# Kernel tuning notes

Measured on AMD Instinct MI355X. Metric: run time of the kernel, lower is better.

## Reference

```python
import jax, jax.numpy as jnp
import numpy as np

EPS = 1e-12  # F.normalize default eps


def setup_inputs() -> dict:
    key = jax.random.key(0)
    k1, k2, k3, k4 = jax.random.split(key, 4)
    B, N, C, NH = 8, 4096, 512, 8
    x = jax.random.normal(k1, (B, N, C), dtype=jnp.float32)
    Wqkv = jax.random.normal(k2, (3 * C, C), dtype=jnp.float32) * 0.02
    Wproj = jax.random.normal(k3, (C, C), dtype=jnp.float32) * 0.02
    bproj = jax.random.normal(k4, (C,), dtype=jnp.float32) * 0.01
    temp = jnp.ones((NH, 1, 1), dtype=jnp.float32)
    return {"x": x, "Wqkv": Wqkv, "Wproj": Wproj, "bproj": bproj,
            "temp": temp, "H": 64, "W": 64}


def _l2norm(t):
    # normalize along last axis, matching F.normalize(p=2, eps=1e-12)
    return t / jnp.maximum(jnp.linalg.norm(t, axis=-1, keepdims=True), EPS)


def reference(x, Wqkv, Wproj, bproj, temp, H, W):
    B, N, C = x.shape
    nh = temp.shape[0]
    hd = C // nh
    # qkv projection: [B, N, 3, nh, hd]
    qkv = jnp.einsum('bnc,dc->bnd', x, Wqkv).reshape(B, N, 3, nh, hd)
    q = qkv[:, :, 0]  # [B, N, nh, hd]
    k = qkv[:, :, 1]
    v = qkv[:, :, 2]
    # transpose to [B, nh, hd, N] and L2-normalize along tokens (N)
    qn = _l2norm(q.transpose(0, 2, 3, 1))
    kn = _l2norm(k.transpose(0, 2, 3, 1))
    vt = v.transpose(0, 2, 3, 1)  # [B, nh, hd, N]
    # channel attention: [B, nh, hd, hd], scaled by learned per-head temp
    attn = jax.nn.softmax(jnp.einsum('bhcn,bhdn->bhcd', qn, kn) * temp, axis=-1)
    # [B, nh, hd, N] -> [B, N, nh, hd] -> [B, N, C]
    out = jnp.einsum('bhcd,bhdn->bhcn', attn, vt).transpose(0, 3, 1, 2).reshape(B, N, C)
    return jnp.einsum('bnc,dc->bnd', out, Wproj) + bproj
```

## Files before the change

### kernel.cpp

```cpp
#include <hip/hip_runtime.h>
#include <stdint.h>

#define DEVI __device__ __forceinline__

typedef __attribute__((ext_vector_type(8))) short bf16x8;
typedef __attribute__((ext_vector_type(4))) float f32x4;
typedef __attribute__((ext_vector_type(4))) unsigned short u16x4;
typedef __attribute__((ext_vector_type(4))) float float4v;

DEVI unsigned short f2bf(float f) {
  unsigned int u = __builtin_bit_cast(unsigned int, f);
  u += 0x7FFFu + ((u >> 16) & 1u);
  return (unsigned short)(u >> 16);
}
DEVI float bf2f(short s) {
  unsigned int u = ((unsigned int)(unsigned short)s) << 16;
  return __builtin_bit_cast(float, u);
}
DEVI void gload16(const unsigned short* g, unsigned short* l) {
  __builtin_amdgcn_global_load_lds(
      (const __attribute__((address_space(1))) unsigned int*)g,
      (__attribute__((address_space(3))) unsigned int*)l, 16, 0, 0);
}

__global__ void cast_prep(const float* __restrict__ x,
                          unsigned short* __restrict__ Xbf,
                          unsigned short* __restrict__ xT,
                          const float* __restrict__ Wqkv,
                          unsigned short* __restrict__ Wqk,
                          unsigned short* __restrict__ WvT) {
  __shared__ float tls[64 * 129];
  const int t = threadIdx.x;
  if (blockIdx.z < 8) {
    const int n0 = blockIdx.x * 128, c0 = blockIdx.y * 64, b = blockIdx.z;
    const int q = t & 15;
    const int nl = t >> 4;
#pragma unroll
    for (int i = 0; i < 8; ++i) {
      const int n = i * 16 + nl;
      const size_t gi = ((size_t)b * 4096 + n0 + n) * 512 + c0 + q * 4;
      float4v f = *(const float4v*)&x[gi];
      u16x4 o;
      o.x = f2bf(f.x); o.y = f2bf(f.y); o.z = f2bf(f.z); o.w = f2bf(f.w);
      *(u16x4*)&Xbf[gi] = o;
      tls[(q * 4 + 0) * 129 + n] = f.x;
      tls[(q * 4 + 1) * 129 + n] = f.y;
      tls[(q * 4 + 2) * 129 + n] = f.z;
      tls[(q * 4 + 3) * 129 + n] = f.w;
    }
    __syncthreads();
    const int cr = t >> 2, nq = t & 3;
#pragma unroll
    for (int ii = 0; ii < 4; ++ii) {
      const int n = nq * 8 + ii * 32;
      bf16x8 o;
#pragma unroll
      for (int s = 0; s < 8; ++s) o[s] = (short)f2bf(tls[cr * 129 + n + s]);
      *(bf16x8*)&xT[((size_t)b * 512 + c0 + cr) * 4096 + n0 + n] = o;
    }
    return;
  }
  const int id = blockIdx.y * 32 + blockIdx.x;
  {
    const float4v* src = (const float4v*)Wqkv;
    u16x4* dst = (u16x4*)Wqk;
    int base = id * 512 + t;
#pragma unroll
    for (int j = 0; j < 2; ++j) {
      int i = base + j * 256;
      float4v f = src[i];
      u16x4 o;
      o.x = f2bf(f.x); o.y = f2bf(f.y); o.z = f2bf(f.z); o.w = f2bf(f.w);
      dst[i] = o;
    }
  }
  if (id < 64) {
    const int tr = id >> 3, tc = id & 7;
    const int c = t & 63, rb = t >> 6;
    __syncthreads();
#pragma unroll
    for (int rr = 0; rr < 16; ++rr) {
      int r = rb * 16 + rr;
      tls[r * 65 + c] = Wqkv[(size_t)(1024 + tr * 64 + r) * 512 + tc * 64 + c];
    }
    __syncthreads();
#pragma unroll
    for (int rr = 0; rr < 16; ++rr) {
      int j = rb * 16 + rr;
      WvT[(size_t)(tc * 64 + j) * 512 + tr * 64 + c] = f2bf(tls[c * 65 + j]);
    }
  }
}

template <int KITERS>
DEVI void gemm_db(const unsigned short* gA, int strideA,
                  const unsigned short* gB, int strideB,
                  unsigned short (*lA)[4096], unsigned short (*lB)[4096],
                  int wave, int wr, int wc, int fr, int kg, f32x4 acc[4][4]) {
  const int wo = wave * 512;
#define STAGE_T(buf, kk)                                                    \
  gload16(gA + (kk) * 32, lA[buf] + wo);                                    \
  gload16(gA + (kk) * 32 + (size_t)64 * strideA, lA[buf] + wo + 2048);      \
  gload16(gB + (kk) * 32, lB[buf] + wo);                                    \
  gload16(gB + (kk) * 32 + (size_t)64 * strideB, lB[buf] + wo + 2048);
  STAGE_T(0, 0);
  __syncthreads();
  int cur = 0;
  for (int kk = 1; kk <= KITERS; ++kk) {
    if (kk < KITERS) { STAGE_T(cur ^ 1, kk); }
    bf16x8 af[4], bfv[4];
#pragma unroll
    for (int mi = 0; mi < 4; ++mi)
      af[mi] = *(const bf16x8*)&lA[cur][(wr * 64 + mi * 16 + fr) * 32 + kg * 8];
#pragma unroll
    for (int ni = 0; ni < 4; ++ni)
      bfv[ni] = *(const bf16x8*)&lB[cur][(wc * 64 + ni * 16 + fr) * 32 + kg * 8];
#pragma unroll
    for (int mi = 0; mi < 4; ++mi)
#pragma unroll
      for (int ni = 0; ni < 4; ++ni)
        acc[mi][ni] = __builtin_amdgcn_mfma_f32_16x16x32_bf16(
            af[mi], bfv[ni], acc[mi][ni], 0, 0, 0);
    __syncthreads();
    cur ^= 1;
  }
#undef STAGE_T
}

__launch_bounds__(256)
__global__ void gsyrk(const unsigned short* __restrict__ xT,
                      unsigned short* __restrict__ Gpart) {
  __shared__ __align__(16) unsigned short lA[2][4096];
  __shared__ __align__(16) unsigned short lB[2][4096];
  static const int PTC[10] = {0, 0, 0, 0, 1, 1, 1, 2, 2, 3};
  static const int PTD[10] = {0, 1, 2, 3, 1, 2, 3, 2, 3, 3};
  const int tid = threadIdx.x, wave = tid >> 6, lane = tid & 63;
  const int wr = wave >> 1, wc = wave & 1, fr = lane & 15, kg = lane >> 4;
  const int tc = PTC[blockIdx.x], td = PTD[blockIdx.x];
  const int chunk = blockIdx.y, b = blockIdx.z;
  const unsigned short* xb = xT + (size_t)b * 512 * 4096 + chunk * 512;
  f32x4 acc[4][4] = {};
  const int sRow = wave * 16 + (lane >> 2);
  const int sK = (lane & 3) * 8;
  gemm_db<16>(xb + (size_t)(tc * 128 + sRow) * 4096 + sK, 4096,
              xb + (size_t)(td * 128 + sRow) * 4096 + sK, 4096,
              lA, lB, wave, wr, wc, fr, kg, acc);
  unsigned short* Gp = Gpart + (size_t)(chunk * 8 + b) * 512 * 512;
#pragma unroll
  for (int mi = 0; mi < 4; ++mi) {
    const int rIT = wr * 64 + mi * 16 + kg * 4;
#pragma unroll
    for (int ni = 0; ni < 4; ++ni) {
      const int cIT = wc * 64 + ni * 16 + fr;
      f32x4 v = acc[mi][ni];
#pragma unroll
      for (int r = 0; r < 4; ++r)
        Gp[(size_t)(tc * 128 + rIT + r) * 512 + td * 128 + cIT] = f2bf(v[r]);
      if (tc != td) {
        u16x4 o;
        o.x = f2bf(v[0]); o.y = f2bf(v[1]); o.z = f2bf(v[2]); o.w = f2bf(v[3]);
        *(u16x4*)&Gp[(size_t)(td * 128 + cIT) * 512 + tc * 128 + rIT] = o;
      }
    }
  }
}

__global__ void greduce(const unsigned short* __restrict__ Gpart,
                        unsigned short* __restrict__ Gbf) {
  const int stride = gridDim.x * blockDim.x;
  const int n4 = 8 * 512 * 512 / 4;
  for (int i = blockIdx.x * blockDim.x + threadIdx.x; i < n4; i += stride) {
    const int b = i >> 16, j4 = i & 65535;
    float s0 = 0, s1 = 0, s2 = 0, s3 = 0;
#pragma unroll
    for (int c = 0; c < 8; ++c) {
      u16x4 v = ((const u16x4*)Gpart)[(size_t)(c * 8 + b) * 65536 + j4];
      s0 += bf2f((short)v.x); s1 += bf2f((short)v.y);
      s2 += bf2f((short)v.z); s3 += bf2f((short)v.w);
    }
    u16x4 o;
    o.x = f2bf(s0); o.y = f2bf(s1); o.z = f2bf(s2); o.w = f2bf(s3);
    ((u16x4*)Gbf)[i] = o;
  }
}

__launch_bounds__(256)
__global__ void tall_gemm(const unsigned short* __restrict__ Wqk,
                          const unsigned short* __restrict__ Gbf,
                          unsigned short* __restrict__ Tbf,
                          float* __restrict__ ssPart) {
  __shared__ __align__(16) unsigned short lA[2][4096];
  __shared__ __align__(16) unsigned short lB[2][4096];
  __shared__ float ssL[128][2];
  const int tid = threadIdx.x, wave = tid >> 6, lane = tid & 63;
  const int wr = wave >> 1, wc = wave & 1, fr = lane & 15, kg = lane >> 4;
  const int rowBase = blockIdx.x * 128, colBase = blockIdx.y * 128;
  const int b = blockIdx.z;
  const unsigned short* Gb = Gbf + (size_t)b * 512 * 512;
  f32x4 acc[4][4] = {};
  const int sRow = wave * 16 + (lane >> 2);
  const int sK = (lane & 3) * 8;
  gemm_db<16>(Wqk + (size_t)(rowBase + sRow) * 512 + sK, 512,
              Gb + (size_t)(colBase + sRow) * 512 + sK, 512,
              lA, lB, wave, wr, wc, fr, kg, acc);
  unsigned short* Tb = Tbf + (size_t)b * 1024 * 512;
#pragma unroll
  for (int mi = 0; mi < 4; ++mi) {
    const int rbase = rowBase + wr * 64 + mi * 16 + kg * 4;
    f32x4 sacc = {0.f, 0.f, 0.f, 0.f};
#pragma unroll
    for (int ni = 0; ni < 4; ++ni) {
      const int col = colBase + wc * 64 + ni * 16 + fr;
      f32x4 v = acc[mi][ni];
#pragma unroll
      for (int r = 0; r < 4; ++r) {
        float w = bf2f((short)Wqk[(size_t)(rbase + r) * 512 + col]);
        Tb[(size_t)(rbase + r) * 512 + col] = f2bf(v[r]);
        sacc[r] += v[r] * w;
      }
    }
#pragma unroll
    for (int o = 1; o < 16; o <<= 1) {
#pragma unroll
      for (int r = 0; r < 4; ++r) sacc[r] += __shfl_xor(sacc[r], o);
    }
    if (fr == 0) {
#pragma unroll
      for (int r = 0; r < 4; ++r)
        ssL[wr * 64 + mi * 16 + kg * 4 + r][wc] = sacc[r];
    }
  }
  __syncthreads();
  if (tid < 128)
    ssPart[((size_t)blockIdx.y * 8 + b) * 1024 + rowBase + tid] =
        ssL[tid][0] + ssL[tid][1];
}

__global__ void s_softmax(const unsigned short* __restrict__ Tbf,
                          const unsigned short* __restrict__ Wqk,
                          const float* __restrict__ ssPart,
                          const float* __restrict__ temp,
                          float* __restrict__ attnOut) {
  __shared__ float Sl[64 * 64];
  __shared__ float invq[64], invk[64];
  const int bh = blockIdx.x, b = bh >> 3, h = bh & 7;
  const unsigned short* qbase = Tbf + (size_t)(b * 1024 + h * 64) * 512;
  const unsigned short* kbase = Wqk + (size_t)(512 + h * 64) * 512;
  const int t = threadIdx.x;
  const int wave = t >> 6, lane = t & 63;
  const int wr = wave >> 1, wc = wave & 1, fr = lane & 15, kg = lane >> 4;
  f32x4 acc[2][2] = {};
  for (int kk = 0; kk < 512; kk += 32) {
    bf16x8 a[2], bb[2];
#pragma unroll
    for (int mi = 0; mi < 2; ++mi)
      a[mi] = *(const bf16x8*)(qbase + (size_t)(wr * 32 + mi * 16 + fr) * 512 + kk + kg * 8);
#pragma unroll
    for (int ni = 0; ni < 2; ++ni)
      bb[ni] = *(const bf16x8*)(kbase + (size_t)(wc * 32 + ni * 16 + fr) * 512 + kk + kg * 8);
#pragma unroll
    for (int mi = 0; mi < 2; ++mi)
#pragma unroll
      for (int ni = 0; ni < 2; ++ni)
        acc[mi][ni] = __builtin_amdgcn_mfma_f32_16x16x32_bf16(a[mi], bb[ni], acc[mi][ni], 0, 0, 0);
  }
#pragma unroll
  for (int mi = 0; mi < 2; ++mi)
#pragma unroll
    for (int ni = 0; ni < 2; ++ni) {
      f32x4 v = acc[mi][ni];
#pragma unroll
      for (int r = 0; r < 4; ++r)
        Sl[(wr * 32 + mi * 16 + kg * 4 + r) * 64 + wc * 32 + ni * 16 + fr] = v[r];
    }
  if (t < 128) {
    const int r = (t >> 6) * 512 + h * 64 + (t & 63);
    float s = 0.f;
#pragma unroll
    for (int nt = 0; nt < 4; ++nt) s += ssPart[((size_t)nt * 8 + b) * 1024 + r];
    float inv = 1.f / fmaxf(sqrtf(s), 1e-12f);
    if (t < 64) invq[t] = inv;
    else invk[t - 64] = inv;
  }
  __syncthreads();
  const float tmp = temp[h];
  const int c = t >> 2, q4 = t & 3;
  float lg[16];
  float mx = -1e30f;
#pragma unroll
  for (int j = 0; j < 16; ++j) {
    const int d = q4 * 16 + j;
    lg[j] = Sl[c * 64 + d] * invq[c] * invk[d] * tmp;
    mx = fmaxf(mx, lg[j]);
  }
  mx = fmaxf(mx, __shfl_xor(mx, 1));
  mx = fmaxf(mx, __shfl_xor(mx, 2));
  float sum = 0.f;
#pragma unroll
  for (int j = 0; j < 16; ++j) {
    lg[j] = __expf(lg[j] - mx);
    sum += lg[j];
  }
  sum += __shfl_xor(sum, 1);
  sum += __shfl_xor(sum, 2);
  const float inv = 1.f / sum;
#pragma unroll
  for (int j = 0; j < 16; ++j)
    attnOut[(size_t)bh * 4096 + c * 64 + q4 * 16 + j] = lg[j] * inv;
}

__global__ void weff_kernel(const float* __restrict__ attn,
                            const float* __restrict__ Wproj,
                            unsigned short* __restrict__ Weff) {
  const int bh = blockIdx.x, eb = blockIdx.y;
  const int b = bh >> 3, h = bh & 7;
  __shared__ float at[64 * 64];
  for (int i = threadIdx.x; i < 4096; i += 256)
    at[i] = attn[(size_t)bh * 4096 + i];
  __syncthreads();
  const int e = eb * 64 + (threadIdx.x >> 2);
  const int dq = threadIdx.x & 3;
  float acc[16] = {};
  const float* wrow = Wproj + (size_t)e * 512 + h * 64;
  for (int c = 0; c < 64; ++c) {
    const float w = wrow[c];
#pragma unroll
    for (int j = 0; j < 16; ++j) acc[j] += w * at[c * 64 + dq * 16 + j];
  }
  unsigned short* outp = Weff + ((size_t)b * 512 + e) * 512 + h * 64 + dq * 16;
#pragma unroll
  for (int j = 0; j < 16; ++j) outp[j] = f2bf(acc[j]);
}

__launch_bounds__(256)
__global__ void wcomb_gemm(const unsigned short* __restrict__ WeffAll,
                           const unsigned short* __restrict__ WvT,
                           unsigned short* __restrict__ WcombAll) {
  __shared__ __align__(16) unsigned short lA[2][4096];
  __shared__ __align__(16) unsigned short lB[2][4096];
  const int tid = threadIdx.x, wave = tid >> 6, lane = tid & 63;
  const int wr = wave >> 1, wc = wave & 1, fr = lane & 15, kg = lane >> 4;
  const int b = blockIdx.z;
  const int rowBase = blockIdx.x * 128, colBase = blockIdx.y * 128;
  const unsigned short* A = WeffAll + (size_t)b * 512 * 512;
  f32x4 acc[4][4] = {};
  const int sRow = wave * 16 + (lane >> 2);
  const int sK = (lane & 3) * 8;
  gemm_db<16>(A + (size_t)(rowBase + sRow) * 512 + sK, 512,
              WvT + (size_t)(colBase + sRow) * 512 + sK, 512,
              lA, lB, wave, wr, wc, fr, kg, acc);
  unsigned short* Wc = WcombAll + (size_t)b * 512 * 512;
#pragma unroll
  for (int mi = 0; mi < 4; ++mi) {
    const int rbase = rowBase + wr * 64 + mi * 16 + kg * 4;
#pragma unroll
    for (int ni = 0; ni < 4; ++ni) {
      const int col = colBase + wc * 64 + ni * 16 + fr;
      f32x4 v = acc[mi][ni];
#pragma unroll
      for (int r = 0; r < 4; ++r)
        Wc[(size_t)(rbase + r) * 512 + col] = f2bf(v[r]);
    }
  }
}

__launch_bounds__(256)
__global__ void out_gemm(const unsigned short* __restrict__ Xbf,
                         const unsigned short* __restrict__ WcombAll,
                         const float* __restrict__ bias,
                         float* __restrict__ out) {
  __shared__ __align__(16) unsigned short lA[2][4096];
  __shared__ __align__(16) unsigned short lB[2][4096];
  const int tid = threadIdx.x, wave = tid >> 6, lane = tid & 63;
  const int wr = wave >> 1, wc = wave & 1, fr = lane & 15, kg = lane >> 4;
  const int b = blockIdx.z;
  const int rowBase = blockIdx.x * 128, colBase = blockIdx.y * 128;
  const unsigned short* A = Xbf + (size_t)b * 4096 * 512;
  const unsigned short* Bw = WcombAll + (size_t)b * 512 * 512;
  f32x4 acc[4][4] = {};
  const int sRow = wave * 16 + (lane >> 2);
  const int sK = (lane & 3) * 8;
  gemm_db<16>(A + (size_t)(rowBase + sRow) * 512 + sK, 512,
              Bw + (size_t)(colBase + sRow) * 512 + sK, 512,
              lA, lB, wave, wr, wc, fr, kg, acc);
#pragma unroll
  for (int mi = 0; mi < 4; ++mi) {
    const int rbase = rowBase + wr * 64 + mi * 16 + kg * 4;
#pragma unroll
    for (int ni = 0; ni < 4; ++ni) {
      const int col = colBase + wc * 64 + ni * 16 + fr;
      const float bcol = bias[col];
      f32x4 v = acc[mi][ni];
#pragma unroll
      for (int r = 0; r < 4; ++r)
        out[((size_t)b * 4096 + rbase + r) * 512 + col] = v[r] + bcol;
    }
  }
}

extern "C" void kernel_launch(void* const* d_in, const int* in_sizes, int n_in,
                              void* d_out, int out_size, void* d_ws, size_t ws_size,
                              hipStream_t stream) {
  const float* x = (const float*)d_in[0];
  const float* Wqkv = (const float*)d_in[1];
  const float* Wproj = (const float*)d_in[2];
  const float* bproj = (const float*)d_in[3];
  const float* temp = (const float*)d_in[4];
  float* out = (float*)d_out;

  char* ws = (char*)d_ws;
  unsigned short* Xbf = (unsigned short*)(ws + 0);
  unsigned short* xT = (unsigned short*)(ws + 33554432);
  unsigned short* Wqk = (unsigned short*)(ws + 67108864);
  unsigned short* WvT = (unsigned short*)(ws + 68157440);
  unsigned short* Gpart = (unsigned short*)(ws + 68681728);
  unsigned short* Gbf = (unsigned short*)(ws + 102236160);
  unsigned short* Tbf = (unsigned short*)(ws + 106430464);
  float* ssPart = (float*)(ws + 114819072);
  float* attn = (float*)(ws + 114950144);
  unsigned short* Weff = (unsigned short*)(ws + 115998720);
  unsigned short* Wcomb = (unsigned short*)(ws + 120193024);

  cast_prep<<<dim3(32, 8, 9), 256, 0, stream>>>(x, Xbf, xT, Wqkv, Wqk, WvT);
  gsyrk<<<dim3(10, 8, 8), 256, 0, stream>>>(xT, Gpart);
  greduce<<<1024, 256, 0, stream>>>(Gpart, Gbf);
  tall_gemm<<<dim3(8, 4, 8), 256, 0, stream>>>(Wqk, Gbf, Tbf, ssPart);
  s_softmax<<<64, 256, 0, stream>>>(Tbf, Wqk, ssPart, temp, attn);
  weff_kernel<<<dim3(64, 8), 256, 0, stream>>>(attn, Wproj, Weff);
  wcomb_gemm<<<dim3(4, 4, 8), 256, 0, stream>>>(Weff, WvT, Wcomb);
  out_gemm<<<dim3(32, 4, 8), 256, 0, stream>>>(Xbf, Wcomb, bproj, out);
}
```

Baseline: 143.0 us.

## Use 256x256 swizzled-LDS GEMM tiles for gsyrk and out_gemm

Adds a shared 256x256-tile, 8-wave GEMM loop with K=64 stages, an XOR-swizzled LDS layout, explicit vmcnt waits and MFMA priority hints. gsyrk and out_gemm now use it. gsyrk drops the symmetric 10-tile triangle scheme and computes all four 256 tiles. The larger tiles raise data reuse per block and the swizzle cuts LDS bank conflicts, but grids shrink to 256 blocks and gsyrk now does redundant work on the symmetric half.

After: 130.4 us. 8.8% less time.

```diff
diff --git a/kernel.cpp b/kernel.cpp
--- a/kernel.cpp
+++ b/kernel.cpp
@@ -89,6 +89,122 @@
       int j = rb * 16 + rr;
       WvT[(size_t)(tc * 64 + j) * 512 + tr * 64 + c] = f2bf(tls[c * 65 + j]);
     }
+  }
+}
+
+#define STAGE256(kt)                                                         \
+  {                                                                          \
+    const int bo_ = ((kt) & 1) * 16384;                                      \
+    _Pragma("unroll") for (int i_ = 0; i_ < 4; ++i_) {                       \
+      gload16(pA + (size_t)i_ * 64 * strideA + (kt) * 64,                    \
+              ldsA + bo_ + i_ * 4096 + wave * 512);                          \
+      gload16(pB + (size_t)i_ * 64 * strideB + (kt) * 64,                    \
+              ldsB + bo_ + i_ * 4096 + wave * 512);                          \
+    }                                                                        \
+  }
+
+template <int NT>
+DEVI void gemm256_loop(const unsigned short* pA, size_t strideA,
+                       const unsigned short* pB, size_t strideB,
+                       unsigned short* ldsA, unsigned short* ldsB,
+                       int wave, int lane, f32x4 acc[8][4]) {
+  const int wr = wave >> 2, wc = wave & 3;
+  const int fr = lane & 15, kg = lane >> 4;
+  const int x0 = ((kg * 16) ^ ((fr & 7) << 4)) >> 1;
+  const int x1 = ((64 + kg * 16) ^ ((fr & 7) << 4)) >> 1;
+  STAGE256(0);
+  for (int kt = 0; kt < NT; ++kt) {
+    __builtin_amdgcn_s_barrier();
+    __builtin_amdgcn_sched_barrier(0);
+    if (kt + 1 < NT) {
+      STAGE256(kt + 1);
+      asm volatile("s_waitcnt vmcnt(8)" ::: "memory");
+    } else {
+      asm volatile("s_waitcnt vmcnt(0)" ::: "memory");
+    }
+    __builtin_amdgcn_sched_barrier(0);
+    __builtin_amdgcn_s_barrier();
+    __builtin_amdgcn_sched_barrier(0);
+    const int bo = (kt & 1) * 16384;
+    bf16x8 bfrag[4][2];
+#pragma unroll
+    for (int n = 0; n < 4; ++n) {
+      const int ro = (wc * 64 + n * 16 + fr) * 64;
+      bfrag[n][0] = *(const bf16x8*)&ldsB[bo + ro + x0];
+      bfrag[n][1] = *(const bf16x8*)&ldsB[bo + ro + x1];
+    }
+#pragma unroll
+    for (int mp = 0; mp < 4; ++mp) {
+      bf16x8 af[2][2];
+#pragma unroll
+      for (int mi = 0; mi < 2; ++mi) {
+        const int ro = (wr * 128 + (mp * 2 + mi) * 16 + fr) * 64;
+        af[mi][0] = *(const bf16x8*)&ldsA[bo + ro + x0];
+        af[mi][1] = *(const bf16x8*)&ldsA[bo + ro + x1];
+      }
+      __builtin_amdgcn_s_setprio(1);
+#pragma unroll
+      for (int mi = 0; mi < 2; ++mi)
+#pragma unroll
+        for (int n = 0; n < 4; ++n) {
+          acc[mp * 2 + mi][n] = __builtin_amdgcn_mfma_f32_16x16x32_bf16(
+              af[mi][0], bfrag[n][0], acc[mp * 2 + mi][n], 0, 0, 0);
+          acc[mp * 2 + mi][n] = __builtin_amdgcn_mfma_f32_16x16x32_bf16(
+              af[mi][1], bfrag[n][1], acc[mp * 2 + mi][n], 0, 0, 0);
+        }
+      __builtin_amdgcn_s_setprio(0);
+    }
+  }
+}
+
+__launch_bounds__(512, 2)
+__global__ void gsyrk(const unsigned short* __restrict__ xT,
+                      unsigned short* __restrict__ Gpart) {
+  __shared__ __align__(16) unsigned short ldsA[2 * 16384];
+  __shared__ __align__(16) unsigned short ldsB[2 * 16384];
+  const int tid = threadIdx.x, wave = tid >> 6, lane = tid & 63;
+  const int tc = blockIdx.x >> 1, td = blockIdx.x & 1;
+  const int chunk = blockIdx.y, b = blockIdx.z;
+  const unsigned short* xb = xT + (size_t)b * 512 * 4096 + chunk * 512;
+  const int sRow = tid >> 3;
+  const int kEl = 8 * ((tid & 7) ^ ((tid >> 3) & 7));
+  const unsigned short* pA = xb + (size_t)(tc * 256 + sRow) * 4096 + kEl;
+  const unsigned short* pB = xb + (size_t)(td * 256 + sRow) * 4096 + kEl;
+  f32x4 acc[8][4] = {};
+  gemm256_loop<8>(pA, 4096, pB, 4096, ldsA, ldsB, wave, lane, acc);
+  const int wr = wave >> 2, wc = wave & 3;
+  const int fr = lane & 15, kg = lane >> 4;
+  unsigned short* Gp = Gpart + (size_t)(chunk * 8 + b) * 512 * 512;
+#pragma unroll
+  for (int m = 0; m < 8; ++m) {
+    const int row0 = tc * 256 + wr * 128 + m * 16 + kg * 4;
+#pragma unroll
+    for (int n = 0; n < 4; ++n) {
+      const int col = td * 256 + wc * 64 + n * 16 + fr;
+      f32x4 v = acc[m][n];
+#pragma unroll
+      for (int r = 0; r < 4; ++r)
+        Gp[(size_t)(row0 + r) * 512 + col] = f2bf(v[r]);
+    }
+  }
+}
+
+__global__ void greduce(const unsigned short* __restrict__ Gpart,
+                        unsigned short* __restrict__ Gbf) {
+  const int stride = gridDim.x * blockDim.x;
+  const int n4 = 8 * 512 * 512 / 4;
+  for (int i = blockIdx.x * blockDim.x + threadIdx.x; i < n4; i += stride) {
+    const int b = i >> 16, j4 = i & 65535;
+    float s0 = 0, s1 = 0, s2 = 0, s3 = 0;
+#pragma unroll
+    for (int c = 0; c < 8; ++c) {
+      u16x4 v = ((const u16x4*)Gpart)[(size_t)(c * 8 + b) * 65536 + j4];
+      s0 += bf2f((short)v.x); s1 += bf2f((short)v.y);
+      s2 += bf2f((short)v.z); s3 += bf2f((short)v.w);
+    }
+    u16x4 o;
+    o.x = f2bf(s0); o.y = f2bf(s1); o.z = f2bf(s2); o.w = f2bf(s3);
+    ((u16x4*)Gbf)[i] = o;
   }
 }
 
@@ -125,63 +241,6 @@
     cur ^= 1;
   }
 #undef STAGE_T
-}
-
-__launch_bounds__(256)
-__global__ void gsyrk(const unsigned short* __restrict__ xT,
-                      unsigned short* __restrict__ Gpart) {
-  __shared__ __align__(16) unsigned short lA[2][4096];
-  __shared__ __align__(16) unsigned short lB[2][4096];
-  static const int PTC[10] = {0, 0, 0, 0, 1, 1, 1, 2, 2, 3};
-  static const int PTD[10] = {0, 1, 2, 3, 1, 2, 3, 2, 3, 3};
-  const int tid = threadIdx.x, wave = tid >> 6, lane = tid & 63;
-  const int wr = wave >> 1, wc = wave & 1, fr = lane & 15, kg = lane >> 4;
-  const int tc = PTC[blockIdx.x], td = PTD[blockIdx.x];
-  const int chunk = blockIdx.y, b = blockIdx.z;
-  const unsigned short* xb = xT + (size_t)b * 512 * 4096 + chunk * 512;
-  f32x4 acc[4][4] = {};
-  const int sRow = wave * 16 + (lane >> 2);
-  const int sK = (lane & 3) * 8;
-  gemm_db<16>(xb + (size_t)(tc * 128 + sRow) * 4096 + sK, 4096,
-              xb + (size_t)(td * 128 + sRow) * 4096 + sK, 4096,
-              lA, lB, wave, wr, wc, fr, kg, acc);
-  unsigned short* Gp = Gpart + (size_t)(chunk * 8 + b) * 512 * 512;
-#pragma unroll
-  for (int mi = 0; mi < 4; ++mi) {
-    const int rIT = wr * 64 + mi * 16 + kg * 4;
-#pragma unroll
-    for (int ni = 0; ni < 4; ++ni) {
-      const int cIT = wc * 64 + ni * 16 + fr;
-      f32x4 v = acc[mi][ni];
-#pragma unroll
-      for (int r = 0; r < 4; ++r)
-        Gp[(size_t)(tc * 128 + rIT + r) * 512 + td * 128 + cIT] = f2bf(v[r]);
-      if (tc != td) {
-        u16x4 o;
-        o.x = f2bf(v[0]); o.y = f2bf(v[1]); o.z = f2bf(v[2]); o.w = f2bf(v[3]);
-        *(u16x4*)&Gp[(size_t)(td * 128 + cIT) * 512 + tc * 128 + rIT] = o;
-      }
-    }
-  }
-}
-
-__global__ void greduce(const unsigned short* __restrict__ Gpart,
-                        unsigned short* __restrict__ Gbf) {
-  const int stride = gridDim.x * blockDim.x;
-  const int n4 = 8 * 512 * 512 / 4;
-  for (int i = blockIdx.x * blockDim.x + threadIdx.x; i < n4; i += stride) {
-    const int b = i >> 16, j4 = i & 65535;
-    float s0 = 0, s1 = 0, s2 = 0, s3 = 0;
-#pragma unroll
-    for (int c = 0; c < 8; ++c) {
-      u16x4 v = ((const u16x4*)Gpart)[(size_t)(c * 8 + b) * 65536 + j4];
-      s0 += bf2f((short)v.x); s1 += bf2f((short)v.y);
-      s2 += bf2f((short)v.z); s3 += bf2f((short)v.w);
-    }
-    u16x4 o;
-    o.x = f2bf(s0); o.y = f2bf(s1); o.z = f2bf(s2); o.w = f2bf(s3);
-    ((u16x4*)Gbf)[i] = o;
-  }
 }
 
 __launch_bounds__(256)
@@ -364,36 +423,37 @@
   }
 }
 
-__launch_bounds__(256)
+__launch_bounds__(512, 2)
 __global__ void out_gemm(const unsigned short* __restrict__ Xbf,
                          const unsigned short* __restrict__ WcombAll,
                          const float* __restrict__ bias,
                          float* __restrict__ out) {
-  __shared__ __align__(16) unsigned short lA[2][4096];
-  __shared__ __align__(16) unsigned short lB[2][4096];
+  __shared__ __align__(16) unsigned short ldsA[2 * 16384];
+  __shared__ __align__(16) unsigned short ldsB[2 * 16384];
   const int tid = threadIdx.x, wave = tid >> 6, lane = tid & 63;
-  const int wr = wave >> 1, wc = wave & 1, fr = lane & 15, kg = lane >> 4;
   const int b = blockIdx.z;
-  const int rowBase = blockIdx.x * 128, colBase = blockIdx.y * 128;
+  const int rowBase = blockIdx.x * 256, colBase = blockIdx.y * 256;
   const unsigned short* A = Xbf + (size_t)b * 4096 * 512;
   const unsigned short* Bw = WcombAll + (size_t)b * 512 * 512;
-  f32x4 acc[4][4] = {};
-  const int sRow = wave * 16 + (lane >> 2);
-  const int sK = (lane & 3) * 8;
-  gemm_db<16>(A + (size_t)(rowBase + sRow) * 512 + sK, 512,
-              Bw + (size_t)(colBase + sRow) * 512 + sK, 512,
-              lA, lB, wave, wr, wc, fr, kg, acc);
-#pragma unroll
-  for (int mi = 0; mi < 4; ++mi) {
-    const int rbase = rowBase + wr * 64 + mi * 16 + kg * 4;
-#pragma unroll
-    for (int ni = 0; ni < 4; ++ni) {
-      const int col = colBase + wc * 64 + ni * 16 + fr;
+  const int sRow = tid >> 3;
+  const int kEl = 8 * ((tid & 7) ^ ((tid >> 3) & 7));
+  const unsigned short* pA = A + (size_t)(rowBase + sRow) * 512 + kEl;
+  const unsigned short* pB = Bw + (size_t)(colBase + sRow) * 512 + kEl;
+  f32x4 acc[8][4] = {};
+  gemm256_loop<8>(pA, 512, pB, 512, ldsA, ldsB, wave, lane, acc);
+  const int wr = wave >> 2, wc = wave & 3;
+  const int fr = lane & 15, kg = lane >> 4;
+#pragma unroll
+  for (int m = 0; m < 8; ++m) {
+    const int row0 = rowBase + wr * 128 + m * 16 + kg * 4;
+#pragma unroll
+    for (int n = 0; n < 4; ++n) {
+      const int col = colBase + wc * 64 + n * 16 + fr;
       const float bcol = bias[col];
-      f32x4 v = acc[mi][ni];
+      f32x4 v = acc[m][n];
 #pragma unroll
       for (int r = 0; r < 4; ++r)
-        out[((size_t)b * 4096 + rbase + r) * 512 + col] = v[r] + bcol;
+        out[((size_t)b * 4096 + row0 + r) * 512 + col] = v[r] + bcol;
     }
   }
 }
@@ -422,11 +482,11 @@
   unsigned short* Wcomb = (unsigned short*)(ws + 120193024);
 
   cast_prep<<<dim3(32, 8, 9), 256, 0, stream>>>(x, Xbf, xT, Wqkv, Wqk, WvT);
-  gsyrk<<<dim3(10, 8, 8), 256, 0, stream>>>(xT, Gpart);
+  gsyrk<<<dim3(4, 8, 8), 512, 0, stream>>>(xT, Gpart);
   greduce<<<1024, 256, 0, stream>>>(Gpart, Gbf);
   tall_gemm<<<dim3(8, 4, 8), 256, 0, stream>>>(Wqk, Gbf, Tbf, ssPart);
   s_softmax<<<64, 256, 0, stream>>>(Tbf, Wqk, ssPart, temp, attn);
   weff_kernel<<<dim3(64, 8), 256, 0, stream>>>(attn, Wproj, Weff);
   wcomb_gemm<<<dim3(4, 4, 8), 256, 0, stream>>>(Weff, WvT, Wcomb);
-  out_gemm<<<dim3(32, 4, 8), 256, 0, stream>>>(Xbf, Wcomb, bproj, out);
-}
+  out_gemm<<<dim3(16, 2, 8), 512, 0, stream>>>(Xbf, Wcomb, bproj, out);
+}
```
